# Kernel optimization log

Hardware: AMD Instinct MI355X
Metric: run time of the kernel (lower is better)

Reference implementation:

```python
import jax, jax.numpy as jnp
import numpy as np

NB_HEAD = 16
SIZE_PER_HEAD = 64
D_MODEL = NB_HEAD * SIZE_PER_HEAD  # 1024
B, S, D_IN = 8, 2048, 1024


def setup_inputs() -> dict:
    key = jax.random.key(0)
    ks = jax.random.split(key, 8)
    def glorot(k, shape):
        lim = np.sqrt(6.0 / (shape[0] + shape[1]))
        return jax.random.uniform(k, shape, jnp.float32, -lim, lim)
    return {
        "Q_seq": jax.random.normal(ks[0], (B, S, D_IN), jnp.float32),
        "K_seq": jax.random.normal(ks[1], (B, S, D_IN), jnp.float32),
        "V_seq": jax.random.normal(ks[2], (B, S, D_IN), jnp.float32),
        "WQ": glorot(ks[3], (D_IN, D_MODEL)),
        "WK": glorot(ks[4], (D_IN, D_MODEL)),
        "Wa": glorot(ks[5], (D_MODEL, NB_HEAD)),
        "Wb": glorot(ks[6], (D_MODEL, NB_HEAD)),
        "WP": glorot(ks[7], (D_MODEL, D_MODEL)),
    }


def reference(Q_seq, K_seq, V_seq, WQ, WK, Wa, Wb, WP):
    # Fastformer additive attention (unmasked 3-input path). V_seq is unused,
    # faithful to the original Keras layer which never reads it.
    b, s, _ = Q_seq.shape
    h, dh = NB_HEAD, SIZE_PER_HEAD
    scale = 1.0 / np.sqrt(dh).astype(np.float32)

    Q = Q_seq @ WQ                                        # [b,s,d]
    # additive query attention logits -> [b,h,s]
    alpha = jax.nn.softmax(jnp.einsum('bsd,de->bes', Q, Wa) * scale, axis=-1)
    Qh = Q.reshape(b, s, h, dh).transpose(0, 2, 1, 3)     # [b,h,s,dh]
    q_glob = jnp.einsum('bhs,bhsd->bhd', alpha, Qh)       # pooled global query

    Kp = (K_seq @ WK).reshape(b, s, h, dh).transpose(0, 2, 1, 3)  # [b,h,s,dh]
    QAK = Kp * q_glob[:, :, None, :]                      # [b,h,s,dh]

    # NOTE: original reshapes [b,h,s,dh] -> [b,s,h*dh] WITHOUT permuting
    # (intentional layout scramble in the source); reproduce exactly.
    QAK_D = QAK.reshape(b, s, h * dh)
    beta = jax.nn.softmax(jnp.einsum('bsd,de->bes', QAK_D, Wb) * scale, axis=-1)
    k_glob = jnp.einsum('bhs,bhsd->bhd', beta, QAK)       # pooled global key [b,h,dh]

    QKQ = k_glob[:, :, None, :] * Qh                      # [b,h,s,dh]
    out = QKQ.transpose(0, 2, 1, 3).reshape(b, s, h * dh) @ WP
    out = out.reshape(b, s, h, dh).transpose(0, 2, 1, 3) + Qh  # residual with Q
    return out.transpose(0, 2, 1, 3).reshape(b, s, h * dh)     # [b,s,d]
```

## Files before the change

kernel.cpp:

```cpp
#include <hip/hip_runtime.h>
#include <stdint.h>

typedef __attribute__((ext_vector_type(8))) short short8;
typedef __attribute__((ext_vector_type(4))) short sh4;
typedef __attribute__((ext_vector_type(4))) float floatx4;
typedef __attribute__((ext_vector_type(4))) unsigned int uintx4;

__device__ __forceinline__ float bs2f(short s) {
  union { unsigned int u; float f; } cv;
  cv.u = ((unsigned int)(unsigned short)s) << 16;
  return cv.f;
}
__device__ __forceinline__ short f2bs(float x) {
  union { float f; unsigned int u; } cv; cv.f = x;
  unsigned int u = cv.u;
  u += 0x7fffu + ((u >> 16) & 1u);
  return (short)(u >> 16);
}
__device__ __forceinline__ unsigned int pack_bf16(float a, float b) {
  unsigned int ua = __float_as_uint(a) + 0x8000u;
  unsigned int ub = __float_as_uint(b) + 0x8000u;
  return __builtin_amdgcn_perm(ub, ua, 0x07060302u);
}
__device__ __forceinline__ void async_copy16(const void* g, void* l) {
  __builtin_amdgcn_global_load_lds(
      (const __attribute__((address_space(1))) void*)g,
      (__attribute__((address_space(3))) void*)l, 16, 0, 0);
}

#define BM 128
#define BN 128
#define BK 64

__device__ __forceinline__ void swizzle_mn(int& m0, int& n0) {
  int flat = blockIdx.x + (blockIdx.y << 3);
  int swz = (flat & 7) * 128 + (flat >> 3);
  n0 = (swz & 7) * BN;
  m0 = (swz >> 3) * BM;
}

__global__ __launch_bounds__(256) void gemm_proj(
    const float* __restrict__ A0, const short* __restrict__ B0,
    short* __restrict__ C0,
    const float* __restrict__ A1, const short* __restrict__ B1,
    short* __restrict__ C1, int N, int K)
{
  __shared__ __align__(16) short As[BM * BK];
  __shared__ __align__(16) short Bs[BN * BK];
  const float* Ap = blockIdx.z ? A1 : A0;
  const short* Bp = blockIdx.z ? B1 : B0;
  short*       Cp = blockIdx.z ? C1 : C0;

  const int tid  = threadIdx.x;
  const int wave = tid >> 6;
  const int lane = tid & 63;
  const int lm = lane & 15, lq = lane >> 4;
  int m0, n0;
  swizzle_mn(m0, n0);
  const int wm = (wave & 1) * 64, wn = (wave >> 1) * 64;

  floatx4 acc[4][4];
#pragma unroll
  for (int r = 0; r < 4; ++r)
#pragma unroll
    for (int c = 0; c < 4; ++c) acc[r][c] = (floatx4)0.0f;

  for (int k0 = 0; k0 < K; k0 += BK) {
    __syncthreads();
#pragma unroll
    for (int it = 0; it < 4; ++it) {
      int chunk = it * 256 + tid;
      int r = chunk >> 3, cc = (chunk & 7) * 8;
      async_copy16(&Bp[(size_t)(n0 + r) * K + k0 + cc], &Bs[r * BK + cc]);
    }
#pragma unroll
    for (int it = 0; it < 4; ++it) {
      int chunk = it * 256 + tid;
      int r = chunk >> 3, cc = (chunk & 7) * 8;
      const float* ap = &Ap[(size_t)(m0 + r) * K + k0 + cc];
      floatx4 f0 = *reinterpret_cast<const floatx4*>(ap);
      floatx4 f1 = *reinterpret_cast<const floatx4*>(ap + 4);
      uintx4 av;
      av[0] = pack_bf16(f0[0], f0[1]); av[1] = pack_bf16(f0[2], f0[3]);
      av[2] = pack_bf16(f1[0], f1[1]); av[3] = pack_bf16(f1[2], f1[3]);
      *reinterpret_cast<uintx4*>(&As[r * BK + cc]) = av;
    }
    __syncthreads();
#pragma unroll
    for (int kk = 0; kk < BK; kk += 32) {
      short8 af[4], bfr[4];
#pragma unroll
      for (int r = 0; r < 4; ++r)
        af[r] = *reinterpret_cast<const short8*>(
            &As[(wm + r * 16 + lm) * BK + kk + lq * 8]);
#pragma unroll
      for (int c = 0; c < 4; ++c)
        bfr[c] = *reinterpret_cast<const short8*>(
            &Bs[(wn + c * 16 + lm) * BK + kk + lq * 8]);
#pragma unroll
      for (int r = 0; r < 4; ++r)
#pragma unroll
        for (int c = 0; c < 4; ++c)
          acc[r][c] = __builtin_amdgcn_mfma_f32_16x16x32_bf16(
              af[r], bfr[c], acc[r][c], 0, 0, 0);
    }
  }

#pragma unroll
  for (int r = 0; r < 4; ++r)
#pragma unroll
    for (int c = 0; c < 4; ++c) {
      int col = n0 + wn + c * 16 + lm;
#pragma unroll
      for (int reg = 0; reg < 4; ++reg) {
        int row = m0 + wm + r * 16 + lq * 4 + reg;
        Cp[(size_t)row * N + col] = f2bs(acc[r][c][reg]);
      }
    }
}

template<int RESID, int OUTF32>
__global__ __launch_bounds__(256) void gemm_bt(
    const short* __restrict__ A, const short* __restrict__ BT,
    void* __restrict__ Cv, const short* __restrict__ resid,
    int M, int N, int K)
{
  __shared__ __align__(16) short As[BM * BK];
  __shared__ __align__(16) short Bs[BN * BK];
  const int tid  = threadIdx.x;
  const int wave = tid >> 6;
  const int lane = tid & 63;
  const int lm   = lane & 15;
  const int lq   = lane >> 4;
  int m0, n0;
  swizzle_mn(m0, n0);
  const int wm = (wave & 1) * 64;
  const int wn = (wave >> 1) * 64;

  floatx4 acc[4][4];
#pragma unroll
  for (int r = 0; r < 4; ++r)
#pragma unroll
    for (int c = 0; c < 4; ++c) acc[r][c] = (floatx4)0.0f;

  for (int k0 = 0; k0 < K; k0 += BK) {
    __syncthreads();
#pragma unroll
    for (int it = 0; it < 4; ++it) {
      int chunk = it * 256 + tid;
      int r = chunk >> 3, cc = (chunk & 7) * 8;
      async_copy16(&BT[(size_t)(n0 + r) * K + k0 + cc], &Bs[r * BK + cc]);
    }
#pragma unroll
    for (int it = 0; it < 4; ++it) {
      int chunk = it * 256 + tid;
      int r = chunk >> 3, cc = (chunk & 7) * 8;
      async_copy16(&A[(size_t)(m0 + r) * K + k0 + cc], &As[r * BK + cc]);
    }
    __syncthreads();
#pragma unroll
    for (int kk = 0; kk < BK; kk += 32) {
      short8 af[4], bfr[4];
#pragma unroll
      for (int r = 0; r < 4; ++r)
        af[r] = *reinterpret_cast<const short8*>(&As[(wm + r * 16 + lm) * BK + kk + lq * 8]);
#pragma unroll
      for (int c = 0; c < 4; ++c)
        bfr[c] = *reinterpret_cast<const short8*>(&Bs[(wn + c * 16 + lm) * BK + kk + lq * 8]);
#pragma unroll
      for (int r = 0; r < 4; ++r)
#pragma unroll
        for (int c = 0; c < 4; ++c)
          acc[r][c] = __builtin_amdgcn_mfma_f32_16x16x32_bf16(af[r], bfr[c], acc[r][c], 0, 0, 0);
    }
  }

#pragma unroll
  for (int r = 0; r < 4; ++r)
#pragma unroll
    for (int c = 0; c < 4; ++c) {
      int col = n0 + wn + c * 16 + lm;
#pragma unroll
      for (int reg = 0; reg < 4; ++reg) {
        int row = m0 + wm + r * 16 + lq * 4 + reg;
        size_t idx = (size_t)row * N + col;
        float v = acc[r][c][reg];
        if (RESID) v += bs2f(resid[idx]);
        if (OUTF32) ((float*)Cv)[idx] = v;
        else        ((short*)Cv)[idx] = f2bs(v);
      }
    }
}

__global__ __launch_bounds__(256) void transpose_cvt3(
    const float* __restrict__ i0, const float* __restrict__ i1,
    const float* __restrict__ i2, short* __restrict__ o0,
    short* __restrict__ o1, short* __restrict__ o2) {
  const float* in = blockIdx.z == 0 ? i0 : (blockIdx.z == 1 ? i1 : i2);
  short* out = blockIdx.z == 0 ? o0 : (blockIdx.z == 1 ? o1 : o2);
  __shared__ short tile[32][33];
  int bx = blockIdx.x * 32, by = blockIdx.y * 32;
  int tx = threadIdx.x & 31;
  int ty = threadIdx.x >> 5;
#pragma unroll
  for (int i = 0; i < 32; i += 8)
    tile[ty + i][tx] = f2bs(in[(size_t)(by + ty + i) * 1024 + bx + tx]);
  __syncthreads();
#pragma unroll
  for (int i = 0; i < 32; i += 8)
    out[(size_t)(bx + ty + i) * 1024 + by + tx] = tile[tx][ty + i];
}

__global__ __launch_bounds__(256) void w_transpose(const float* __restrict__ Wa,
                                                   const float* __restrict__ Wb,
                                                   short* __restrict__ WaB,
                                                   short* __restrict__ WbB) {
  int idx = blockIdx.x * 256 + threadIdx.x;
  const float* src = idx < 16384 ? Wa : Wb;
  short* dst = idx < 16384 ? WaB : WbB;
  int i = idx & 16383;
  int e = i >> 10, k = i & 1023;
  dst[i] = f2bs(src[k * 16 + e]);
}

template<int SCRAMBLE>
__global__ __launch_bounds__(64) void skinny_logits(
    const short* __restrict__ X, const short* __restrict__ WB,
    const float* __restrict__ qg, float* __restrict__ out)
{
  const int lane = threadIdx.x;
  const int lm = lane & 15, lq = lane >> 4;
  const int blk = blockIdx.x;
  const int b = blk >> 7;
  const int s0 = (blk & 127) * 16;
  floatx4 acc = (floatx4)0.0f;
  const short* b0 = WB + lm * 1024 + lq * 8;

  if (!SCRAMBLE) {
    const short* a0 = X + ((size_t)(b * 2048 + s0 + lm)) * 1024 + lq * 8;
#pragma unroll 16
    for (int c = 0; c < 32; ++c) {
      short8 a  = *reinterpret_cast<const short8*>(a0 + c * 32);
      short8 bf = *reinterpret_cast<const short8*>(b0 + c * 32);
      acc = __builtin_amdgcn_mfma_f32_16x16x32_bf16(a, bf, acc, 0, 0, 0);
    }
  } else {
    const int h = s0 >> 7, t0 = s0 & 127;
    const float* qgp = qg + b * 1024 + h * 64;
    const short* xb = X + ((size_t)(b * 2048 + (t0 + lm) * 16)) * 1024 + h * 64;
#pragma unroll 16
    for (int c = 0; c < 32; ++c) {
      int dp = c * 32 + lq * 8;
      int u = dp >> 6, j0 = dp & 63;
      short8 a = *reinterpret_cast<const short8*>(xb + (size_t)u * 1024 + j0);
      floatx4 g0 = *reinterpret_cast<const floatx4*>(qgp + j0);
      floatx4 g1 = *reinterpret_cast<const floatx4*>(qgp + j0 + 4);
      uintx4 av;
      av[0] = pack_bf16(bs2f(a[0]) * g0[0], bs2f(a[1]) * g0[1]);
      av[1] = pack_bf16(bs2f(a[2]) * g0[2], bs2f(a[3]) * g0[3]);
      av[2] = pack_bf16(bs2f(a[4]) * g1[0], bs2f(a[5]) * g1[1]);
      av[3] = pack_bf16(bs2f(a[6]) * g1[2], bs2f(a[7]) * g1[3]);
      short8 as = __builtin_bit_cast(short8, av);
      short8 bf = *reinterpret_cast<const short8*>(b0 + c * 32);
      acc = __builtin_amdgcn_mfma_f32_16x16x32_bf16(as, bf, acc, 0, 0, 0);
    }
  }
  float* o = out + ((size_t)(b * 16 + lm)) * 2048 + s0 + lq * 4;
  floatx4 r;
#pragma unroll
  for (int i = 0; i < 4; ++i) r[i] = __expf(acc[i] * 0.125f);
  *reinterpret_cast<floatx4*>(o) = r;
}

__global__ __launch_bounds__(256) void pool_partial(const float* __restrict__ ew,
                                                    const short* __restrict__ X,
                                                    float* __restrict__ part,
                                                    float* __restrict__ psum) {
  __shared__ float p[16][32];
  int blk = blockIdx.x, b = blk >> 6, sc = blk & 63, s0 = sc * 32;
  int tid = threadIdx.x;
  {
    int h = tid >> 4, ss = (tid & 15) * 2;
    const float* pr = ew + (size_t)(b * 16 + h) * 2048 + s0 + ss;
    p[h][ss] = pr[0]; p[h][ss + 1] = pr[1];
  }
  __syncthreads();
  if (tid < 16) {
    float s = 0.f;
#pragma unroll
    for (int j = 0; j < 32; ++j) s += p[tid][j];
    psum[blk * 16 + tid] = s;
  }
  int d = tid * 4, h = tid >> 4;
  float a0 = 0, a1 = 0, a2 = 0, a3 = 0;
  const short* Xp = X + ((size_t)b * 2048 + s0) * 1024 + d;
#pragma unroll 4
  for (int s = 0; s < 32; ++s) {
    sh4 x = *reinterpret_cast<const sh4*>(Xp + (size_t)s * 1024);
    float w = p[h][s];
    a0 += w * bs2f(x[0]); a1 += w * bs2f(x[1]);
    a2 += w * bs2f(x[2]); a3 += w * bs2f(x[3]);
  }
  float* o = part + (size_t)blk * 1024 + d;
  o[0] = a0; o[1] = a1; o[2] = a2; o[3] = a3;
}

template<int SCALE>
__global__ __launch_bounds__(256) void pool_reduce(const float* __restrict__ part,
                                                   const float* __restrict__ psum,
                                                   const float* __restrict__ g,
                                                   float* __restrict__ out) {
  int b = blockIdx.x, d = threadIdx.x * 4, h = threadIdx.x >> 4;
  float a0 = 0, a1 = 0, a2 = 0, a3 = 0, hs = 0;
  for (int sc = 0; sc < 64; ++sc) {
    const float* pp = part + (size_t)(b * 64 + sc) * 1024 + d;
    a0 += pp[0]; a1 += pp[1]; a2 += pp[2]; a3 += pp[3];
    hs += psum[(b * 64 + sc) * 16 + h];
  }
  float inv = 1.0f / hs;
  a0 *= inv; a1 *= inv; a2 *= inv; a3 *= inv;
  if (SCALE) {
    const float* gp = g + b * 1024 + d;
    a0 *= gp[0]; a1 *= gp[1]; a2 *= gp[2]; a3 *= gp[3];
  }
  float* op = out + b * 1024 + d;
  op[0] = a0; op[1] = a1; op[2] = a2; op[3] = a3;
}

__global__ __launch_bounds__(256) void scale_a(const short* __restrict__ Qb,
                                               const float* __restrict__ g,
                                               short* __restrict__ QG) {
  size_t base = ((size_t)blockIdx.x * 256 + threadIdx.x) * 8;
  int b = (int)(base >> 21), d = (int)(base & 1023);
  short8 v = *reinterpret_cast<const short8*>(&Qb[base]);
  const float* gp = g + b * 1024 + d;
#pragma unroll
  for (int e = 0; e < 8; ++e) v[e] = f2bs(bs2f(v[e]) * gp[e]);
  *reinterpret_cast<short8*>(&QG[base]) = v;
}

extern "C" void kernel_launch(void* const* d_in, const int* in_sizes, int n_in,
                              void* d_out, int out_size, void* d_ws, size_t ws_size,
                              hipStream_t stream) {
  (void)in_sizes; (void)n_in; (void)out_size; (void)ws_size;
  const float* Qseq = (const float*)d_in[0];
  const float* Kseq = (const float*)d_in[1];
  const float* WQ = (const float*)d_in[3];
  const float* WK = (const float*)d_in[4];
  const float* Wa = (const float*)d_in[5];
  const float* Wb = (const float*)d_in[6];
  const float* WP = (const float*)d_in[7];
  float* outp = (float*)d_out;

  char* ws = (char*)d_ws;
  const size_t MB = 1024 * 1024;
  short* Qb   = (short*)(ws + 0);
  short* Kb   = (short*)(ws + 32 * MB);
  short* WQT  = (short*)(ws + 64 * MB);
  short* WKT  = (short*)(ws + 66 * MB);
  short* WPT  = (short*)(ws + 68 * MB);
  float* la   = (float*)(ws + 70 * MB);
  float* lb   = (float*)(ws + 71 * MB);
  float* qg   = (float*)(ws + 72 * MB);
  float* gv   = (float*)(ws + 72 * MB + 64 * 1024);
  short* WaB  = (short*)(ws + 72 * MB + 128 * 1024);
  short* WbB  = (short*)(ws + 72 * MB + 192 * 1024);
  float* part = (float*)(ws + 73 * MB);
  float* psum = (float*)(ws + 75 * MB);
  short* QG   = Kb;

  dim3 tb(256);
  transpose_cvt3<<<dim3(32, 32, 3), tb, 0, stream>>>(WQ, WK, WP, WQT, WKT, WPT);
  w_transpose<<<128, tb, 0, stream>>>(Wa, Wb, WaB, WbB);

  gemm_proj<<<dim3(8, 128, 2), tb, 0, stream>>>(
      Qseq, WQT, Qb, Kseq, WKT, Kb, 1024, 1024);

  skinny_logits<0><<<1024, 64, 0, stream>>>(Qb, WaB, nullptr, la);
  pool_partial<<<512, tb, 0, stream>>>(la, Qb, part, psum);
  pool_reduce<0><<<8, tb, 0, stream>>>(part, psum, nullptr, qg);

  skinny_logits<1><<<1024, 64, 0, stream>>>(Kb, WbB, qg, lb);
  pool_partial<<<512, tb, 0, stream>>>(lb, Kb, part, psum);
  pool_reduce<1><<<8, tb, 0, stream>>>(part, psum, qg, gv);

  scale_a<<<8192, tb, 0, stream>>>(Qb, gv, QG);
  gemm_bt<1, 1><<<dim3(8, 128), tb, 0, stream>>>(QG, WPT, outp, Qb, 16384, 1024, 1024);
}
```

Measured before the change: 441.5 us.

## Use 256x256 double-buffered GEMM tiles and fuse gate scaling into output GEMM

Both projection GEMMs move to 256x256 tiles with 512 threads and double-buffered LDS. The next K-slice is prefetched while the current one is computed, so there is one barrier per iteration. The separate scale_a kernel is removed: the output GEMM multiplies Q by the per-batch gate vector while packing its A tile. This cuts one full read-write pass over a 32MB buffer and one launch. The cost is 128KB of LDS per block and high register pressure from 8x4 accumulators plus prefetch registers, which may limit occupancy to one block per CU.

```diff
diff --git a/kernel.cpp b/kernel.cpp
--- a/kernel.cpp
+++ b/kernel.cpp
@@ -28,166 +28,225 @@
       (__attribute__((address_space(3))) void*)l, 16, 0, 0);
 }
 
-#define BM 128
-#define BN 128
-#define BK 64
-
-__device__ __forceinline__ void swizzle_mn(int& m0, int& n0) {
-  int flat = blockIdx.x + (blockIdx.y << 3);
-  int swz = (flat & 7) * 128 + (flat >> 3);
-  n0 = (swz & 7) * BN;
-  m0 = (swz >> 3) * BM;
-}
-
-__global__ __launch_bounds__(256) void gemm_proj(
+#define PBM 256
+#define PBN 256
+#define PBK 64
+#define PNT 16
+
+__device__ __forceinline__ void swizzle_mn256(int& m0, int& n0) {
+  int flat = blockIdx.x + (blockIdx.y << 2);
+  int swz = (flat & 7) * 32 + (flat >> 3);
+  n0 = (swz & 3) * PBN;
+  m0 = (swz >> 2) * PBM;
+}
+
+__global__ __launch_bounds__(512) void gemm_proj(
     const float* __restrict__ A0, const short* __restrict__ B0,
     short* __restrict__ C0,
     const float* __restrict__ A1, const short* __restrict__ B1,
     short* __restrict__ C1, int N, int K)
 {
-  __shared__ __align__(16) short As[BM * BK];
-  __shared__ __align__(16) short Bs[BN * BK];
+  __shared__ __align__(16) short As[2][PBM * PBK];
+  __shared__ __align__(16) short Bs[2][PBN * PBK];
   const float* Ap = blockIdx.z ? A1 : A0;
   const short* Bp = blockIdx.z ? B1 : B0;
   short*       Cp = blockIdx.z ? C1 : C0;
 
-  const int tid  = threadIdx.x;
-  const int wave = tid >> 6;
-  const int lane = tid & 63;
+  const int tid = threadIdx.x;
+  const int wave = tid >> 6, lane = tid & 63;
   const int lm = lane & 15, lq = lane >> 4;
+  const int wr = wave >> 2, wc = wave & 3;
   int m0, n0;
-  swizzle_mn(m0, n0);
-  const int wm = (wave & 1) * 64, wn = (wave >> 1) * 64;
-
-  floatx4 acc[4][4];
-#pragma unroll
-  for (int r = 0; r < 4; ++r)
+  swizzle_mn256(m0, n0);
+  const int r8 = tid >> 3, cc = (tid & 7) * 8;
+
+  floatx4 acc[8][4];
+#pragma unroll
+  for (int r = 0; r < 8; ++r)
 #pragma unroll
     for (int c = 0; c < 4; ++c) acc[r][c] = (floatx4)0.0f;
 
-  for (int k0 = 0; k0 < K; k0 += BK) {
-    __syncthreads();
+  floatx4 pa[4][2];
+
+  auto stageB = [&](int buf, int kb) {
 #pragma unroll
     for (int it = 0; it < 4; ++it) {
-      int chunk = it * 256 + tid;
-      int r = chunk >> 3, cc = (chunk & 7) * 8;
-      async_copy16(&Bp[(size_t)(n0 + r) * K + k0 + cc], &Bs[r * BK + cc]);
-    }
+      int r = it * 64 + r8;
+      async_copy16(&Bp[(size_t)(n0 + r) * K + kb + cc], &Bs[buf][r * PBK + cc]);
+    }
+  };
+  auto loadA = [&](int kb) {
 #pragma unroll
     for (int it = 0; it < 4; ++it) {
-      int chunk = it * 256 + tid;
-      int r = chunk >> 3, cc = (chunk & 7) * 8;
-      const float* ap = &Ap[(size_t)(m0 + r) * K + k0 + cc];
-      floatx4 f0 = *reinterpret_cast<const floatx4*>(ap);
-      floatx4 f1 = *reinterpret_cast<const floatx4*>(ap + 4);
+      const float* ap = Ap + (size_t)(m0 + it * 64 + r8) * K + kb + cc;
+      pa[it][0] = *reinterpret_cast<const floatx4*>(ap);
+      pa[it][1] = *reinterpret_cast<const floatx4*>(ap + 4);
+    }
+  };
+  auto packA = [&](int buf) {
+#pragma unroll
+    for (int it = 0; it < 4; ++it) {
       uintx4 av;
-      av[0] = pack_bf16(f0[0], f0[1]); av[1] = pack_bf16(f0[2], f0[3]);
-      av[2] = pack_bf16(f1[0], f1[1]); av[3] = pack_bf16(f1[2], f1[3]);
-      *reinterpret_cast<uintx4*>(&As[r * BK + cc]) = av;
-    }
-    __syncthreads();
-#pragma unroll
-    for (int kk = 0; kk < BK; kk += 32) {
-      short8 af[4], bfr[4];
-#pragma unroll
-      for (int r = 0; r < 4; ++r)
+      av[0] = pack_bf16(pa[it][0][0], pa[it][0][1]);
+      av[1] = pack_bf16(pa[it][0][2], pa[it][0][3]);
+      av[2] = pack_bf16(pa[it][1][0], pa[it][1][1]);
+      av[3] = pack_bf16(pa[it][1][2], pa[it][1][3]);
+      *reinterpret_cast<uintx4*>(&As[buf][(it * 64 + r8) * PBK + cc]) = av;
+    }
+  };
+  auto compute = [&](int buf) {
+#pragma unroll
+    for (int kk = 0; kk < PBK; kk += 32) {
+      short8 af[8], bfr[4];
+#pragma unroll
+      for (int r = 0; r < 8; ++r)
         af[r] = *reinterpret_cast<const short8*>(
-            &As[(wm + r * 16 + lm) * BK + kk + lq * 8]);
+            &As[buf][(wr * 128 + r * 16 + lm) * PBK + kk + lq * 8]);
 #pragma unroll
       for (int c = 0; c < 4; ++c)
         bfr[c] = *reinterpret_cast<const short8*>(
-            &Bs[(wn + c * 16 + lm) * BK + kk + lq * 8]);
-#pragma unroll
-      for (int r = 0; r < 4; ++r)
+            &Bs[buf][(wc * 64 + c * 16 + lm) * PBK + kk + lq * 8]);
+#pragma unroll
+      for (int r = 0; r < 8; ++r)
 #pragma unroll
         for (int c = 0; c < 4; ++c)
           acc[r][c] = __builtin_amdgcn_mfma_f32_16x16x32_bf16(
               af[r], bfr[c], acc[r][c], 0, 0, 0);
     }
-  }
-
-#pragma unroll
-  for (int r = 0; r < 4; ++r)
+  };
+
+  stageB(0, 0);
+  loadA(0);
+  packA(0);
+  __syncthreads();
+
+  int cur = 0;
+  for (int t = 0; t < PNT - 1; ++t) {
+    const int nxt = cur ^ 1;
+    const int kb = (t + 1) * PBK;
+    stageB(nxt, kb);
+    loadA(kb);
+    compute(cur);
+    packA(nxt);
+    __syncthreads();
+    cur = nxt;
+  }
+  compute(cur);
+
+#pragma unroll
+  for (int r = 0; r < 8; ++r)
 #pragma unroll
     for (int c = 0; c < 4; ++c) {
-      int col = n0 + wn + c * 16 + lm;
+      int col = n0 + wc * 64 + c * 16 + lm;
 #pragma unroll
       for (int reg = 0; reg < 4; ++reg) {
-        int row = m0 + wm + r * 16 + lq * 4 + reg;
+        int row = m0 + wr * 128 + r * 16 + lq * 4 + reg;
         Cp[(size_t)row * N + col] = f2bs(acc[r][c][reg]);
       }
     }
 }
 
-template<int RESID, int OUTF32>
-__global__ __launch_bounds__(256) void gemm_bt(
-    const short* __restrict__ A, const short* __restrict__ BT,
-    void* __restrict__ Cv, const short* __restrict__ resid,
-    int M, int N, int K)
+__global__ __launch_bounds__(512) void gemm_out(
+    const short* __restrict__ Aq, const float* __restrict__ gvp,
+    const short* __restrict__ BT, float* __restrict__ Cv,
+    const short* __restrict__ resid, int N, int K)
 {
-  __shared__ __align__(16) short As[BM * BK];
-  __shared__ __align__(16) short Bs[BN * BK];
-  const int tid  = threadIdx.x;
-  const int wave = tid >> 6;
-  const int lane = tid & 63;
-  const int lm   = lane & 15;
-  const int lq   = lane >> 4;
+  __shared__ __align__(16) short As[2][PBM * PBK];
+  __shared__ __align__(16) short Bs[2][PBN * PBK];
+
+  const int tid = threadIdx.x;
+  const int wave = tid >> 6, lane = tid & 63;
+  const int lm = lane & 15, lq = lane >> 4;
+  const int wr = wave >> 2, wc = wave & 3;
   int m0, n0;
-  swizzle_mn(m0, n0);
-  const int wm = (wave & 1) * 64;
-  const int wn = (wave >> 1) * 64;
-
-  floatx4 acc[4][4];
-#pragma unroll
-  for (int r = 0; r < 4; ++r)
+  swizzle_mn256(m0, n0);
+  const int r8 = tid >> 3, cc = (tid & 7) * 8;
+  const int bq = m0 >> 11;
+
+  floatx4 acc[8][4];
+#pragma unroll
+  for (int r = 0; r < 8; ++r)
 #pragma unroll
     for (int c = 0; c < 4; ++c) acc[r][c] = (floatx4)0.0f;
 
-  for (int k0 = 0; k0 < K; k0 += BK) {
+  short8 qa[4];
+  floatx4 g0, g1;
+
+  auto stageB = [&](int buf, int kb) {
+#pragma unroll
+    for (int it = 0; it < 4; ++it) {
+      int r = it * 64 + r8;
+      async_copy16(&BT[(size_t)(n0 + r) * K + kb + cc], &Bs[buf][r * PBK + cc]);
+    }
+  };
+  auto loadA = [&](int kb) {
+#pragma unroll
+    for (int it = 0; it < 4; ++it)
+      qa[it] = *reinterpret_cast<const short8*>(
+          &Aq[(size_t)(m0 + it * 64 + r8) * K + kb + cc]);
+    g0 = *reinterpret_cast<const floatx4*>(gvp + bq * 1024 + kb + cc);
+    g1 = *reinterpret_cast<const floatx4*>(gvp + bq * 1024 + kb + cc + 4);
+  };
+  auto packA = [&](int buf) {
+#pragma unroll
+    for (int it = 0; it < 4; ++it) {
+      uintx4 av;
+      av[0] = pack_bf16(bs2f(qa[it][0]) * g0[0], bs2f(qa[it][1]) * g0[1]);
+      av[1] = pack_bf16(bs2f(qa[it][2]) * g0[2], bs2f(qa[it][3]) * g0[3]);
+      av[2] = pack_bf16(bs2f(qa[it][4]) * g1[0], bs2f(qa[it][5]) * g1[1]);
+      av[3] = pack_bf16(bs2f(qa[it][6]) * g1[2], bs2f(qa[it][7]) * g1[3]);
+      *reinterpret_cast<uintx4*>(&As[buf][(it * 64 + r8) * PBK + cc]) = av;
+    }
+  };
+  auto compute = [&](int buf) {
+#pragma unroll
+    for (int kk = 0; kk < PBK; kk += 32) {
+      short8 af[8], bfr[4];
+#pragma unroll
+      for (int r = 0; r < 8; ++r)
+        af[r] = *reinterpret_cast<const short8*>(
+            &As[buf][(wr * 128 + r * 16 + lm) * PBK + kk + lq * 8]);
+#pragma unroll
+      for (int c = 0; c < 4; ++c)
+        bfr[c] = *reinterpret_cast<const short8*>(
+            &Bs[buf][(wc * 64 + c * 16 + lm) * PBK + kk + lq * 8]);
+#pragma unroll
+      for (int r = 0; r < 8; ++r)
+#pragma unroll
+        for (int c = 0; c < 4; ++c)
+          acc[r][c] = __builtin_amdgcn_mfma_f32_16x16x32_bf16(
+              af[r], bfr[c], acc[r][c], 0, 0, 0);
+    }
+  };
+
+  stageB(0, 0);
+  loadA(0);
+  packA(0);
+  __syncthreads();
+
+  int cur = 0;
+  for (int t = 0; t < PNT - 1; ++t) {
+    const int nxt = cur ^ 1;
+    const int kb = (t + 1) * PBK;
+    stageB(nxt, kb);
+    loadA(kb);
+    compute(cur);
+    packA(nxt);
     __syncthreads();
-#pragma unroll
-    for (int it = 0; it < 4; ++it) {
-      int chunk = it * 256 + tid;
-      int r = chunk >> 3, cc = (chunk & 7) * 8;
-      async_copy16(&BT[(size_t)(n0 + r) * K + k0 + cc], &Bs[r * BK + cc]);
-    }
-#pragma unroll
-    for (int it = 0; it < 4; ++it) {
-      int chunk = it * 256 + tid;
-      int r = chunk >> 3, cc = (chunk & 7) * 8;
-      async_copy16(&A[(size_t)(m0 + r) * K + k0 + cc], &As[r * BK + cc]);
-    }
-    __syncthreads();
-#pragma unroll
-    for (int kk = 0; kk < BK; kk += 32) {
-      short8 af[4], bfr[4];
-#pragma unroll
-      for (int r = 0; r < 4; ++r)
-        af[r] = *reinterpret_cast<const short8*>(&As[(wm + r * 16 + lm) * BK + kk + lq * 8]);
-#pragma unroll
-      for (int c = 0; c < 4; ++c)
-        bfr[c] = *reinterpret_cast<const short8*>(&Bs[(wn + c * 16 + lm) * BK + kk + lq * 8]);
-#pragma unroll
-      for (int r = 0; r < 4; ++r)
-#pragma unroll
-        for (int c = 0; c < 4; ++c)
-          acc[r][c] = __builtin_amdgcn_mfma_f32_16x16x32_bf16(af[r], bfr[c], acc[r][c], 0, 0, 0);
-    }
-  }
-
-#pragma unroll
-  for (int r = 0; r < 4; ++r)
+    cur = nxt;
+  }
+  compute(cur);
+
+#pragma unroll
+  for (int r = 0; r < 8; ++r)
 #pragma unroll
     for (int c = 0; c < 4; ++c) {
-      int col = n0 + wn + c * 16 + lm;
+      int col = n0 + wc * 64 + c * 16 + lm;
 #pragma unroll
       for (int reg = 0; reg < 4; ++reg) {
-        int row = m0 + wm + r * 16 + lq * 4 + reg;
+        int row = m0 + wr * 128 + r * 16 + lq * 4 + reg;
         size_t idx = (size_t)row * N + col;
-        float v = acc[r][c][reg];
-        if (RESID) v += bs2f(resid[idx]);
-        if (OUTF32) ((float*)Cv)[idx] = v;
-        else        ((short*)Cv)[idx] = f2bs(v);
+        Cv[idx] = acc[r][c][reg] + bs2f(resid[idx]);
       }
     }
 }
@@ -327,18 +386,6 @@
   op[0] = a0; op[1] = a1; op[2] = a2; op[3] = a3;
 }
 
-__global__ __launch_bounds__(256) void scale_a(const short* __restrict__ Qb,
-                                               const float* __restrict__ g,
-                                               short* __restrict__ QG) {
-  size_t base = ((size_t)blockIdx.x * 256 + threadIdx.x) * 8;
-  int b = (int)(base >> 21), d = (int)(base & 1023);
-  short8 v = *reinterpret_cast<const short8*>(&Qb[base]);
-  const float* gp = g + b * 1024 + d;
-#pragma unroll
-  for (int e = 0; e < 8; ++e) v[e] = f2bs(bs2f(v[e]) * gp[e]);
-  *reinterpret_cast<short8*>(&QG[base]) = v;
-}
-
 extern "C" void kernel_launch(void* const* d_in, const int* in_sizes, int n_in,
                               void* d_out, int out_size, void* d_ws, size_t ws_size,
                               hipStream_t stream) {
@@ -367,13 +414,12 @@
   short* WbB  = (short*)(ws + 72 * MB + 192 * 1024);
   float* part = (float*)(ws + 73 * MB);
   float* psum = (float*)(ws + 75 * MB);
-  short* QG   = Kb;
 
   dim3 tb(256);
   transpose_cvt3<<<dim3(32, 32, 3), tb, 0, stream>>>(WQ, WK, WP, WQT, WKT, WPT);
   w_transpose<<<128, tb, 0, stream>>>(Wa, Wb, WaB, WbB);
 
-  gemm_proj<<<dim3(8, 128, 2), tb, 0, stream>>>(
+  gemm_proj<<<dim3(4, 64, 2), dim3(512), 0, stream>>>(
       Qseq, WQT, Qb, Kseq, WKT, Kb, 1024, 1024);
 
   skinny_logits<0><<<1024, 64, 0, stream>>>(Qb, WaB, nullptr, la);
@@ -384,6 +430,6 @@
   pool_partial<<<512, tb, 0, stream>>>(lb, Kb, part, psum);
   pool_reduce<1><<<8, tb, 0, stream>>>(part, psum, qg, gv);
 
-  scale_a<<<8192, tb, 0, stream>>>(Qb, gv, QG);
-  gemm_bt<1, 1><<<dim3(8, 128), tb, 0, stream>>>(QG, WPT, outp, Qb, 16384, 1024, 1024);
-}
+  gemm_out<<<dim3(4, 64), dim3(512), 0, stream>>>(
+      Qb, gv, WPT, outp, Qb, 1024, 1024);
+}
```

New measurement: 419.5 us. 1.05x faster.

## Replace GEMMs with triple-buffered 256x128 pipelined kernel and fold gate into weights

Applied to the files above, without the earlier changes.

Both GEMMs now run in a single templated kernel with 512 threads, 256x128 tiles, triple-buffered LDS fed by async global-to-LDS loads, explicit vmcnt waits and XOR-swizzled LDS layout to avoid bank conflicts. The fp32 A operand is prefetched into registers and packed to bf16 while the previous tile computes. The per-batch gate k_glob is now folded into a per-batch scaled copy of WP (8 small matrices) instead of scaling the whole Q activation, so the final GEMM reads Qb directly. This adds about 96KB of LDS, which lowers occupancy.

```diff
diff --git a/kernel.cpp b/kernel.cpp
--- a/kernel.cpp
+++ b/kernel.cpp
@@ -28,36 +28,44 @@
       (__attribute__((address_space(3))) void*)l, 16, 0, 0);
 }
 
-#define BM 128
-#define BN 128
-#define BK 64
-
-__device__ __forceinline__ void swizzle_mn(int& m0, int& n0) {
+#define WAIT_VM(N) asm volatile("s_waitcnt vmcnt(" #N ")" ::: "memory")
+#define BAR() asm volatile("s_waitcnt lgkmcnt(0)\ns_barrier" ::: "memory")
+
+#define GBM 256
+#define GBN 128
+#define GBK 64
+#define GNT 16
+
+__device__ __forceinline__ void swizzle_mn_p(int& m0, int& n0) {
   int flat = blockIdx.x + (blockIdx.y << 3);
-  int swz = (flat & 7) * 128 + (flat >> 3);
-  n0 = (swz & 7) * BN;
-  m0 = (swz >> 3) * BM;
-}
-
-__global__ __launch_bounds__(256) void gemm_proj(
-    const float* __restrict__ A0, const short* __restrict__ B0,
-    short* __restrict__ C0,
-    const float* __restrict__ A1, const short* __restrict__ B1,
-    short* __restrict__ C1, int N, int K)
+  int swz = (flat & 7) * 64 + (flat >> 3);
+  n0 = (swz & 7) * GBN;
+  m0 = (swz >> 3) * GBM;
+}
+
+template<int AFP32, int OUTF32, int RESID, int PBB>
+__global__ __launch_bounds__(512) void gemm_pipe(
+    const void* __restrict__ A0, const void* __restrict__ A1,
+    const short* __restrict__ B0, const short* __restrict__ B1,
+    void* __restrict__ C0, void* __restrict__ C1,
+    const short* __restrict__ resid, int N, int K)
 {
-  __shared__ __align__(16) short As[BM * BK];
-  __shared__ __align__(16) short Bs[BN * BK];
-  const float* Ap = blockIdx.z ? A1 : A0;
-  const short* Bp = blockIdx.z ? B1 : B0;
-  short*       Cp = blockIdx.z ? C1 : C0;
-
-  const int tid  = threadIdx.x;
-  const int wave = tid >> 6;
-  const int lane = tid & 63;
+  __shared__ __align__(16) short As[3][GBM * GBK];
+  __shared__ __align__(16) short Bs[3][GBN * GBK];
+
+  const void*  Avp = blockIdx.z ? A1 : A0;
+  const short* Bp  = blockIdx.z ? B1 : B0;
+  void*        Cp  = blockIdx.z ? C1 : C0;
+
+  const int tid = threadIdx.x;
+  const int wave = tid >> 6, lane = tid & 63;
   const int lm = lane & 15, lq = lane >> 4;
+  const int wm = (wave >> 1) * 64;
+  const int wn = (wave & 1) * 64;
   int m0, n0;
-  swizzle_mn(m0, n0);
-  const int wm = (wave & 1) * 64, wn = (wave >> 1) * 64;
+  swizzle_mn_p(m0, n0);
+  if (PBB) Bp += (size_t)(m0 >> 11) * (1024 * 1024);
+  const int r8 = tid >> 3, g = tid & 7;
 
   floatx4 acc[4][4];
 #pragma unroll
@@ -65,115 +73,107 @@
 #pragma unroll
     for (int c = 0; c < 4; ++c) acc[r][c] = (floatx4)0.0f;
 
-  for (int k0 = 0; k0 < K; k0 += BK) {
-    __syncthreads();
+  floatx4 pa[4][2];
+
+  auto stageB = [&](int buf, int kb) {
+#pragma unroll
+    for (int it = 0; it < 2; ++it) {
+      int row = it * 64 + r8;
+      async_copy16(&Bp[(size_t)(n0 + row) * K + kb + ((g ^ (row & 7)) << 3)],
+                   &Bs[buf][row * GBK + g * 8]);
+    }
+  };
+  auto stageAb = [&](int buf, int kb) {
+    const short* Ab = (const short*)Avp;
 #pragma unroll
     for (int it = 0; it < 4; ++it) {
-      int chunk = it * 256 + tid;
-      int r = chunk >> 3, cc = (chunk & 7) * 8;
-      async_copy16(&Bp[(size_t)(n0 + r) * K + k0 + cc], &Bs[r * BK + cc]);
-    }
+      int row = it * 64 + r8;
+      async_copy16(&Ab[(size_t)(m0 + row) * K + kb + ((g ^ (row & 7)) << 3)],
+                   &As[buf][row * GBK + g * 8]);
+    }
+  };
+  auto loadA = [&](int kb) {
+    const float* Af = (const float*)Avp;
 #pragma unroll
     for (int it = 0; it < 4; ++it) {
-      int chunk = it * 256 + tid;
-      int r = chunk >> 3, cc = (chunk & 7) * 8;
-      const float* ap = &Ap[(size_t)(m0 + r) * K + k0 + cc];
-      floatx4 f0 = *reinterpret_cast<const floatx4*>(ap);
-      floatx4 f1 = *reinterpret_cast<const floatx4*>(ap + 4);
+      const float* ap = Af + (size_t)(m0 + it * 64 + r8) * K + kb + g * 8;
+      pa[it][0] = *reinterpret_cast<const floatx4*>(ap);
+      pa[it][1] = *reinterpret_cast<const floatx4*>(ap + 4);
+    }
+  };
+  auto packA = [&](int buf) {
+#pragma unroll
+    for (int it = 0; it < 4; ++it) {
+      int row = it * 64 + r8;
+      int slot = g ^ (row & 7);
       uintx4 av;
-      av[0] = pack_bf16(f0[0], f0[1]); av[1] = pack_bf16(f0[2], f0[3]);
-      av[2] = pack_bf16(f1[0], f1[1]); av[3] = pack_bf16(f1[2], f1[3]);
-      *reinterpret_cast<uintx4*>(&As[r * BK + cc]) = av;
-    }
-    __syncthreads();
-#pragma unroll
-    for (int kk = 0; kk < BK; kk += 32) {
-      short8 af[4], bfr[4];
+      av[0] = pack_bf16(pa[it][0][0], pa[it][0][1]);
+      av[1] = pack_bf16(pa[it][0][2], pa[it][0][3]);
+      av[2] = pack_bf16(pa[it][1][0], pa[it][1][1]);
+      av[3] = pack_bf16(pa[it][1][2], pa[it][1][3]);
+      *reinterpret_cast<uintx4*>(&As[buf][row * GBK + slot * 8]) = av;
+    }
+  };
+  auto compute = [&](int buf) {
+#pragma unroll
+    for (int kk = 0; kk < 2; ++kk) {
+      short8 af[4], bfv[4];
+      const int slotx = (kk * 4 + lq) ^ (lm & 7);
 #pragma unroll
       for (int r = 0; r < 4; ++r)
         af[r] = *reinterpret_cast<const short8*>(
-            &As[(wm + r * 16 + lm) * BK + kk + lq * 8]);
+            &As[buf][(wm + r * 16 + lm) * GBK + slotx * 8]);
 #pragma unroll
       for (int c = 0; c < 4; ++c)
-        bfr[c] = *reinterpret_cast<const short8*>(
-            &Bs[(wn + c * 16 + lm) * BK + kk + lq * 8]);
+        bfv[c] = *reinterpret_cast<const short8*>(
+            &Bs[buf][(wn + c * 16 + lm) * GBK + slotx * 8]);
 #pragma unroll
       for (int r = 0; r < 4; ++r)
 #pragma unroll
         for (int c = 0; c < 4; ++c)
           acc[r][c] = __builtin_amdgcn_mfma_f32_16x16x32_bf16(
-              af[r], bfr[c], acc[r][c], 0, 0, 0);
-    }
-  }
-
-#pragma unroll
-  for (int r = 0; r < 4; ++r)
-#pragma unroll
-    for (int c = 0; c < 4; ++c) {
-      int col = n0 + wn + c * 16 + lm;
-#pragma unroll
-      for (int reg = 0; reg < 4; ++reg) {
-        int row = m0 + wm + r * 16 + lq * 4 + reg;
-        Cp[(size_t)row * N + col] = f2bs(acc[r][c][reg]);
-      }
-    }
-}
-
-template<int RESID, int OUTF32>
-__global__ __launch_bounds__(256) void gemm_bt(
-    const short* __restrict__ A, const short* __restrict__ BT,
-    void* __restrict__ Cv, const short* __restrict__ resid,
-    int M, int N, int K)
-{
-  __shared__ __align__(16) short As[BM * BK];
-  __shared__ __align__(16) short Bs[BN * BK];
-  const int tid  = threadIdx.x;
-  const int wave = tid >> 6;
-  const int lane = tid & 63;
-  const int lm   = lane & 15;
-  const int lq   = lane >> 4;
-  int m0, n0;
-  swizzle_mn(m0, n0);
-  const int wm = (wave & 1) * 64;
-  const int wn = (wave >> 1) * 64;
-
-  floatx4 acc[4][4];
-#pragma unroll
-  for (int r = 0; r < 4; ++r)
-#pragma unroll
-    for (int c = 0; c < 4; ++c) acc[r][c] = (floatx4)0.0f;
-
-  for (int k0 = 0; k0 < K; k0 += BK) {
-    __syncthreads();
-#pragma unroll
-    for (int it = 0; it < 4; ++it) {
-      int chunk = it * 256 + tid;
-      int r = chunk >> 3, cc = (chunk & 7) * 8;
-      async_copy16(&BT[(size_t)(n0 + r) * K + k0 + cc], &Bs[r * BK + cc]);
-    }
-#pragma unroll
-    for (int it = 0; it < 4; ++it) {
-      int chunk = it * 256 + tid;
-      int r = chunk >> 3, cc = (chunk & 7) * 8;
-      async_copy16(&A[(size_t)(m0 + r) * K + k0 + cc], &As[r * BK + cc]);
-    }
-    __syncthreads();
-#pragma unroll
-    for (int kk = 0; kk < BK; kk += 32) {
-      short8 af[4], bfr[4];
-#pragma unroll
-      for (int r = 0; r < 4; ++r)
-        af[r] = *reinterpret_cast<const short8*>(&As[(wm + r * 16 + lm) * BK + kk + lq * 8]);
-#pragma unroll
-      for (int c = 0; c < 4; ++c)
-        bfr[c] = *reinterpret_cast<const short8*>(&Bs[(wn + c * 16 + lm) * BK + kk + lq * 8]);
-#pragma unroll
-      for (int r = 0; r < 4; ++r)
-#pragma unroll
-        for (int c = 0; c < 4; ++c)
-          acc[r][c] = __builtin_amdgcn_mfma_f32_16x16x32_bf16(af[r], bfr[c], acc[r][c], 0, 0, 0);
-    }
-  }
+              af[r], bfv[c], acc[r][c], 0, 0, 0);
+    }
+  };
+
+  if (AFP32) {
+    loadA(0); stageB(0, 0);
+    WAIT_VM(2);
+    packA(0);
+    loadA(GBK); stageB(1, GBK);
+    WAIT_VM(2);
+    packA(1);
+  } else {
+    stageAb(0, 0);  stageB(0, 0);
+    stageAb(1, GBK); stageB(1, GBK);
+    WAIT_VM(6);
+  }
+  BAR();
+
+  int cur = 0, stg = 2;
+  for (int u = 0; u < GNT - 2; ++u) {
+    const int kb = (u + 2) * GBK;
+    if (AFP32) {
+      loadA(kb);
+      stageB(stg, kb);
+      compute(cur);
+      WAIT_VM(2);
+      packA(stg);
+    } else {
+      stageAb(stg, kb);
+      stageB(stg, kb);
+      compute(cur);
+      WAIT_VM(6);
+    }
+    BAR();
+    cur = (cur == 2) ? 0 : cur + 1;
+    stg = (stg == 2) ? 0 : stg + 1;
+  }
+  compute(cur);
+  WAIT_VM(0);
+  BAR();
+  cur = (cur == 2) ? 0 : cur + 1;
+  compute(cur);
 
 #pragma unroll
   for (int r = 0; r < 4; ++r)
@@ -186,8 +186,8 @@
         size_t idx = (size_t)row * N + col;
         float v = acc[r][c][reg];
         if (RESID) v += bs2f(resid[idx]);
-        if (OUTF32) ((float*)Cv)[idx] = v;
-        else        ((short*)Cv)[idx] = f2bs(v);
+        if (OUTF32) ((float*)Cp)[idx] = v;
+        else        ((short*)Cp)[idx] = f2bs(v);
       }
     }
 }
@@ -221,6 +221,21 @@
   int i = idx & 16383;
   int e = i >> 10, k = i & 1023;
   dst[i] = f2bs(src[k * 16 + e]);
+}
+
+__global__ __launch_bounds__(256) void wp_scale(const short* __restrict__ WPT,
+                                                const float* __restrict__ gv,
+                                                short* __restrict__ WPg) {
+  size_t idx = ((size_t)blockIdx.x * 256 + threadIdx.x) * 8;
+  int b = (int)(idx >> 20);
+  int nk = (int)(idx & 1048575);
+  int k = nk & 1023;
+  short8 w = *reinterpret_cast<const short8*>(&WPT[nk]);
+  const float* gp = gv + b * 1024 + k;
+  short8 o;
+#pragma unroll
+  for (int e = 0; e < 8; ++e) o[e] = f2bs(bs2f(w[e]) * gp[e]);
+  *reinterpret_cast<short8*>(&WPg[idx]) = o;
 }
 
 template<int SCRAMBLE>
@@ -327,18 +342,6 @@
   op[0] = a0; op[1] = a1; op[2] = a2; op[3] = a3;
 }
 
-__global__ __launch_bounds__(256) void scale_a(const short* __restrict__ Qb,
-                                               const float* __restrict__ g,
-                                               short* __restrict__ QG) {
-  size_t base = ((size_t)blockIdx.x * 256 + threadIdx.x) * 8;
-  int b = (int)(base >> 21), d = (int)(base & 1023);
-  short8 v = *reinterpret_cast<const short8*>(&Qb[base]);
-  const float* gp = g + b * 1024 + d;
-#pragma unroll
-  for (int e = 0; e < 8; ++e) v[e] = f2bs(bs2f(v[e]) * gp[e]);
-  *reinterpret_cast<short8*>(&QG[base]) = v;
-}
-
 extern "C" void kernel_launch(void* const* d_in, const int* in_sizes, int n_in,
                               void* d_out, int out_size, void* d_ws, size_t ws_size,
                               hipStream_t stream) {
@@ -367,14 +370,14 @@
   short* WbB  = (short*)(ws + 72 * MB + 192 * 1024);
   float* part = (float*)(ws + 73 * MB);
   float* psum = (float*)(ws + 75 * MB);
-  short* QG   = Kb;
+  short* WPg  = Kb;
 
   dim3 tb(256);
   transpose_cvt3<<<dim3(32, 32, 3), tb, 0, stream>>>(WQ, WK, WP, WQT, WKT, WPT);
   w_transpose<<<128, tb, 0, stream>>>(Wa, Wb, WaB, WbB);
 
-  gemm_proj<<<dim3(8, 128, 2), tb, 0, stream>>>(
-      Qseq, WQT, Qb, Kseq, WKT, Kb, 1024, 1024);
+  gemm_pipe<1, 0, 0, 0><<<dim3(8, 64, 2), dim3(512), 0, stream>>>(
+      Qseq, Kseq, WQT, WKT, Qb, Kb, nullptr, 1024, 1024);
 
   skinny_logits<0><<<1024, 64, 0, stream>>>(Qb, WaB, nullptr, la);
   pool_partial<<<512, tb, 0, stream>>>(la, Qb, part, psum);
@@ -384,6 +387,7 @@
   pool_partial<<<512, tb, 0, stream>>>(lb, Kb, part, psum);
   pool_reduce<1><<<8, tb, 0, stream>>>(part, psum, qg, gv);
 
-  scale_a<<<8192, tb, 0, stream>>>(Qb, gv, QG);
-  gemm_bt<1, 1><<<dim3(8, 128), tb, 0, stream>>>(QG, WPT, outp, Qb, 16384, 1024, 1024);
-}
+  wp_scale<<<4096, tb, 0, stream>>>(WPT, gv, WPg);
+  gemm_pipe<0, 1, 1, 1><<<dim3(8, 64, 1), dim3(512), 0, stream>>>(
+      Qb, Qb, WPg, WPg, outp, outp, Qb, 1024, 1024);
+}
```

Result: slower. 454.1 us (+2.9%).
